# Performance work log

Hardware: AMD Instinct MI355X
Metric: run time of the kernel (lower is better)

Reference implementation:

```python
import jax, jax.numpy as jnp
import numpy as np

VOCAB, EMBED, HIDDEN, LAYERS = 256, 256, 1024, 2
B, T = 128, 256


def gru_layer(x_seq, h0, W_ih, W_hh, b_ih, b_hh):
    """PyTorch-semantics GRU layer. x_seq:[B,T,in], h0:[B,H] -> ([B,T,H], [B,H]).
    n = tanh(W_in x + b_in + r * (W_hn h + b_hn)); h' = (1-z)*n + z*h.
    Input-gate GEMM is hoisted out of the scan (one big matmul over all T)."""
    H = h0.shape[-1]
    gi = jnp.einsum('bti,gi->btg', x_seq, W_ih) + b_ih  # [B,T,3H]
    gi = jnp.transpose(gi, (1, 0, 2))                   # [T,B,3H] scan over time

    def step(h, gi_t):
        gh = h @ W_hh.T + b_hh                          # [B,3H]
        i_r, i_z, i_n = jnp.split(gi_t, 3, axis=-1)
        h_r, h_z, h_n = jnp.split(gh, 3, axis=-1)
        r = jax.nn.sigmoid(i_r + h_r)
        z = jax.nn.sigmoid(i_z + h_z)
        n = jnp.tanh(i_n + r * h_n)
        h_new = (1.0 - z) * n + z * h
        return h_new, h_new

    h_last, ys = jax.lax.scan(step, h0, gi)
    return jnp.transpose(ys, (1, 0, 2)), h_last         # [B,T,H], [B,H]


def setup_inputs() -> dict:
    key = jax.random.key(0)
    ks = jax.random.split(key, 16)
    s = 1.0 / np.sqrt(HIDDEN)
    u = lambda k, shape: jax.random.uniform(k, shape, jnp.float32, -s, s)
    inp = {
        'x': jax.random.randint(ks[0], (B, T), 0, VOCAB),
        'h0': jax.random.normal(ks[1], (LAYERS, B, HIDDEN), jnp.float32),
        'emb': jax.random.normal(ks[2], (VOCAB, EMBED), jnp.float32),
        'W_ih0': u(ks[3], (3 * HIDDEN, EMBED)),
        'W_hh0': u(ks[4], (3 * HIDDEN, HIDDEN)),
        'b_ih0': u(ks[5], (3 * HIDDEN,)),
        'b_hh0': u(ks[6], (3 * HIDDEN,)),
        'W_ih1': u(ks[7], (3 * HIDDEN, HIDDEN)),
        'W_hh1': u(ks[8], (3 * HIDDEN, HIDDEN)),
        'b_ih1': u(ks[9], (3 * HIDDEN,)),
        'b_hh1': u(ks[10], (3 * HIDDEN,)),
        'fc_W': u(ks[11], (VOCAB, HIDDEN)),
        'fc_b': u(ks[12], (VOCAB,)),
    }
    return inp


def reference(x, h0, emb, W_ih0, W_hh0, b_ih0, b_hh0, W_ih1, W_hh1, b_ih1, b_hh1, fc_W, fc_b):
    xe = emb[x]                                          # [B,T,E]
    y0, h_last0 = gru_layer(xe, h0[0], W_ih0, W_hh0, b_ih0, b_hh0)
    y1, h_last1 = gru_layer(y0, h0[1], W_ih1, W_hh1, b_ih1, b_hh1)
    logits = y1[:, -1, :] @ fc_W.T + fc_b                # [B,VOCAB]
    h = jnp.stack([h_last0, h_last1], axis=0)            # [LAYERS,B,H]
    return logits, h
```

## Files before the change

### kernel.cpp

```cpp
#include <hip/hip_runtime.h>
#include <hip/hip_bf16.h>

using bf16x8 = __attribute__((ext_vector_type(8))) __bf16;
using short8 = __attribute__((ext_vector_type(8))) short;
using f32x4  = __attribute__((ext_vector_type(4))) float;
using f4     = __attribute__((ext_vector_type(4))) float;
using i32x4  = __attribute__((ext_vector_type(4))) int;

constexpr int NB = 128;
constexpr int NT = 256;
constexpr int NH = 1024;
constexpr int NE = 256;
constexpr int NV = 256;

constexpr int WHH_BYTES = 48 * 2048;
constexpr int GH_FLOATS = 24 * 256;
constexpr int NBLK = 256;

__device__ __forceinline__ void ldg_sc(i32x4& d, const void* p) {
  asm volatile("global_load_dwordx4 %0, %1, off sc0 sc1" : "=v"(d) : "v"(p));
}
__device__ __forceinline__ void stg_sc(void* p, i32x4 v) {
  asm volatile("global_store_dwordx4 %0, %1, off sc0 sc1" :: "v"(p), "v"(v) : "memory");
}
__device__ __forceinline__ void vm0_fence() {
  asm volatile("s_waitcnt vmcnt(0)" ::: "memory");
}
__device__ __forceinline__ void use_dep(i32x4& d) {
  asm volatile("" : "+v"(d));
}

__device__ __forceinline__ bf16x8 cvt8(const float* p) {
  short8 r;
  #pragma unroll
  for (int j = 0; j < 8; ++j)
    r[j] = (short)__bfloat16_as_ushort(__float2bfloat16(p[j]));
  return __builtin_bit_cast(bf16x8, r);
}

__global__ __launch_bounds__(256) void embcvt_kernel(const float* __restrict__ e,
                                                     __hip_bfloat16* __restrict__ o) {
  int i = blockIdx.x * 256 + threadIdx.x;
  o[i] = __float2bfloat16(e[i]);
}

template<int LAYER>
__global__ __launch_bounds__(384) void gru_kernel(
    const int* __restrict__ x,
    const __hip_bfloat16* __restrict__ embb,
    const float* __restrict__ Wih,
    const float* __restrict__ Whh,
    const float* __restrict__ bih,
    const float* __restrict__ bhh,
    const float* __restrict__ h0,
    const __hip_bfloat16* __restrict__ yin,
    __hip_bfloat16* __restrict__ yout,
    __hip_bfloat16* __restrict__ hbuf,
    float* __restrict__ hout,
    unsigned int* __restrict__ flags)
{
  extern __shared__ char smem[];
  char*  sWhh  = smem;
  float* sGh   = (float*)(smem + WHH_BYTES);
  float* sBias = sGh + GH_FLOATS;
  char*  sH    = (char*)(sBias + 64);

  const int tid  = threadIdx.x;
  const int lane = tid & 63;
  const int wv   = tid >> 6;
  const int mt   = wv & 1;
  const int ks   = wv >> 1;
  const int b    = blockIdx.x;
  const int rb   = (b >> 1) & 3;
  const int cidx = (b & 1) * 32 + (b >> 3);
  const int r0   = rb * 32;
  const int c0   = cidx * 16;
  unsigned int* pf = flags + rb * 64 * 16;
  const int slot = cidx;
  const int l16  = lane & 15;
  const int lk8  = (lane >> 4) * 8;

  for (int it = 0; it < 16; ++it) {
    int idx = it * 384 + tid;
    int gr = idx >> 7, kc = idx & 127;
    int grow = (gr >> 4) * NH + c0 + (gr & 15);
    short8 v = __builtin_bit_cast(short8, cvt8(Whh + grow * NH + kc * 8));
    *(short8*)(sWhh + ((gr * 2048 + kc * 16) ^ ((gr & 7) << 4))) = v;
  }
  if (tid < 16)       sBias[tid] = bih[c0 + tid] + bhh[c0 + tid];
  else if (tid < 32)  { int c = NH + c0 + tid - 16;   sBias[tid] = bih[c] + bhh[c]; }
  else if (tid < 48)  { int c = 2*NH + c0 + tid - 32; sBias[tid] = bih[c]; }
  else if (tid < 64)  { int c = 2*NH + c0 + tid - 48; sBias[tid] = bhh[c]; }

  constexpr int NFRAG = (LAYER == 0) ? 8 : 32;
  constexpr int KIN   = (LAYER == 0) ? NE : NH;
  bf16x8 wreg[NFRAG];
  #pragma unroll
  for (int kf = 0; kf < NFRAG; ++kf) {
    int grow = ks * NH + c0 + l16;
    wreg[kf] = cvt8(Wih + grow * KIN + kf * 32 + lk8);
  }

  float hown[2] = {0.f, 0.f};
  #pragma unroll
  for (int ei = 0; ei < 2; ++ei) {
    int e = tid + ei * 384;
    if (e < 512) {
      float hv = h0[(r0 + (e >> 4)) * NH + c0 + (e & 15)];
      hown[ei] = hv;
      ((unsigned short*)sH)[e] = __bfloat16_as_ushort(__float2bfloat16(hv));
    }
  }
  __syncthreads();
  if (tid < 64) {
    i32x4 hv = *(const i32x4*)(sH + (tid >> 1) * 32 + (tid & 1) * 16);
    stg_sc(hbuf + (r0 + (tid >> 1)) * NH + c0 + (tid & 1) * 8, hv);
    vm0_fence();
    if (tid == 0)
      __hip_atomic_store(pf + slot * 16, 1u, __ATOMIC_RELAXED,
                         __HIP_MEMORY_SCOPE_AGENT);
  }

  for (int t = 0; t < NT; ++t) {
    const __hip_bfloat16* rbuf = hbuf + (t & 1) * (NB * NH);
    __hip_bfloat16* wbuf = hbuf + ((t + 1) & 1) * (NB * NH);
    const int arow = r0 + mt * 16 + l16;
    const int bxor = (l16 & 7) << 4;
    float* abase = sGh + (lane >> 4) * 64 + l16;

    constexpr int P1 = (LAYER == 0) ? 4 : 24;
    f32x4 ai = {0.f, 0.f, 0.f, 0.f};
    const __hip_bfloat16* xptr;
    if constexpr (LAYER == 0) {
      int xid = x[arow * NT + t];
      xptr = embb + xid * NE + lk8;
    } else {
      xptr = yin + (arow * NT + t) * NH + lk8;
    }
    #pragma unroll
    for (int kk = 0; kk < P1; ++kk) {
      bf16x8 a = __builtin_bit_cast(bf16x8, *(const short8*)(xptr + kk * 32));
      ai = __builtin_amdgcn_mfma_f32_16x16x32_bf16(a, wreg[kk], ai, 0, 0, 0);
    }

    {
      unsigned int ep = (unsigned int)(t + 1);
      if (tid < 64) {
        const unsigned int* f = pf + tid * 16;
        while (__hip_atomic_load(f, __ATOMIC_RELAXED,
                                 __HIP_MEMORY_SCOPE_AGENT) < ep)
          __builtin_amdgcn_s_sleep(1);
      }
      __syncthreads();
    }

    const int nk = (ks < 2) ? 11 : 10;
    const __hip_bfloat16* aptr = rbuf + arow * NH + lk8;
    i32x4 fr[11];
    #pragma unroll
    for (int i = 0; i < 11; ++i)
      if (i < nk) ldg_sc(fr[i], aptr + (ks + 3 * i) * 32);

    #pragma unroll
    for (int kk = P1; kk < NFRAG; ++kk) {
      bf16x8 a = __builtin_bit_cast(bf16x8, *(const short8*)(xptr + kk * 32));
      ai = __builtin_amdgcn_mfma_f32_16x16x32_bf16(a, wreg[kk], ai, 0, 0, 0);
    }
    {
      float* p = abase + (18 + mt * 3 + ks) * 256;
      p[0] = ai[0]; p[16] = ai[1]; p[32] = ai[2]; p[48] = ai[3];
    }

    vm0_fence();
    #pragma unroll
    for (int i = 0; i < 11; ++i)
      if (i < nk) use_dep(fr[i]);
    {
      f32x4 ah0 = {0.f,0.f,0.f,0.f}, ah1 = {0.f,0.f,0.f,0.f}, ah2 = {0.f,0.f,0.f,0.f};
      const int bb0 = (l16)      * 2048 + lk8 * 2;
      const int bb1 = (16 + l16) * 2048 + lk8 * 2;
      const int bb2 = (32 + l16) * 2048 + lk8 * 2;
      #pragma unroll
      for (int i = 0; i < 11; ++i) {
        if (i < nk) {
          int kk = ks + 3 * i;
          bf16x8 a = __builtin_bit_cast(bf16x8, fr[i]);
          bf16x8 b0 = __builtin_bit_cast(bf16x8,
              *(const short8*)(sWhh + ((bb0 + kk * 64) ^ bxor)));
          ah0 = __builtin_amdgcn_mfma_f32_16x16x32_bf16(a, b0, ah0, 0, 0, 0);
          bf16x8 b1 = __builtin_bit_cast(bf16x8,
              *(const short8*)(sWhh + ((bb1 + kk * 64) ^ bxor)));
          ah1 = __builtin_amdgcn_mfma_f32_16x16x32_bf16(a, b1, ah1, 0, 0, 0);
          bf16x8 b2 = __builtin_bit_cast(bf16x8,
              *(const short8*)(sWhh + ((bb2 + kk * 64) ^ bxor)));
          ah2 = __builtin_amdgcn_mfma_f32_16x16x32_bf16(a, b2, ah2, 0, 0, 0);
        }
      }
      float* p0 = abase + (ks * 6 + mt * 3 + 0) * 256;
      float* p1 = abase + (ks * 6 + mt * 3 + 1) * 256;
      float* p2 = abase + (ks * 6 + mt * 3 + 2) * 256;
      p0[0] = ah0[0]; p0[16] = ah0[1]; p0[32] = ah0[2]; p0[48] = ah0[3];
      p1[0] = ah1[0]; p1[16] = ah1[1]; p1[32] = ah1[2]; p1[48] = ah1[3];
      p2[0] = ah2[0]; p2[16] = ah2[1]; p2[32] = ah2[2]; p2[48] = ah2[3];
    }
    __syncthreads();

    #pragma unroll
    for (int ei = 0; ei < 2; ++ei) {
      int e = tid + ei * 384;
      if (e < 512) {
        int lrow = e >> 4, lcol = e & 15;
        int m2 = lrow >> 4, off = (lrow & 15) * 16 + lcol;
        float ghr = sGh[(0*6 + m2*3 + 0) * 256 + off]
                  + sGh[(1*6 + m2*3 + 0) * 256 + off]
                  + sGh[(2*6 + m2*3 + 0) * 256 + off];
        float ghz = sGh[(0*6 + m2*3 + 1) * 256 + off]
                  + sGh[(1*6 + m2*3 + 1) * 256 + off]
                  + sGh[(2*6 + m2*3 + 1) * 256 + off];
        float ghn = sGh[(0*6 + m2*3 + 2) * 256 + off]
                  + sGh[(1*6 + m2*3 + 2) * 256 + off]
                  + sGh[(2*6 + m2*3 + 2) * 256 + off];
        float gir = sGh[(18 + m2*3 + 0) * 256 + off];
        float giz = sGh[(18 + m2*3 + 1) * 256 + off];
        float gin = sGh[(18 + m2*3 + 2) * 256 + off];
        float r = 1.f / (1.f + __expf(-(gir + ghr + sBias[lcol])));
        float z = 1.f / (1.f + __expf(-(giz + ghz + sBias[16 + lcol])));
        float npre = (gin + sBias[32 + lcol]) + r * (ghn + sBias[48 + lcol]);
        float n = 2.f / (1.f + __expf(-2.f * npre)) - 1.f;
        float hn = (1.f - z) * n + z * hown[ei];
        hown[ei] = hn;
        __hip_bfloat16 hb = __float2bfloat16(hn);
        ((unsigned short*)sH)[e] = __bfloat16_as_ushort(hb);
        if constexpr (LAYER == 0)
          yout[((r0 + lrow) * NT + t) * NH + c0 + lcol] = hb;
      }
    }

    __syncthreads();
    if (tid < 64) {
      i32x4 hv = *(const i32x4*)(sH + (tid >> 1) * 32 + (tid & 1) * 16);
      stg_sc(wbuf + (r0 + (tid >> 1)) * NH + c0 + (tid & 1) * 8, hv);
      vm0_fence();
      if (tid == 0)
        __hip_atomic_store(pf + slot * 16, (unsigned int)(t + 2),
                           __ATOMIC_RELAXED, __HIP_MEMORY_SCOPE_AGENT);
    }
  }

  #pragma unroll
  for (int ei = 0; ei < 2; ++ei) {
    int e = tid + ei * 384;
    if (e < 512) {
      int lrow = e >> 4, lcol = e & 15;
      hout[(r0 + lrow) * NH + c0 + lcol] = hown[ei];
    }
  }
}

__global__ __launch_bounds__(256) void logits_kernel(
    const __hip_bfloat16* __restrict__ h1,
    const float* __restrict__ fcW,
    const float* __restrict__ fcb,
    float* __restrict__ out)
{
  __shared__ float hrow[NH];
  int b = blockIdx.x, v = threadIdx.x;
  if (v < 128) {
    i32x4 hv;
    ldg_sc(hv, h1 + b * NH + v * 8);
    vm0_fence();
    use_dep(hv);
    short8 s = __builtin_bit_cast(short8, hv);
    #pragma unroll
    for (int j = 0; j < 8; ++j) {
      union { unsigned int i; float f; } c;
      c.i = ((unsigned int)(unsigned short)s[j]) << 16;
      hrow[v * 8 + j] = c.f;
    }
  }
  __syncthreads();
  float acc = fcb[v];
  for (int k = 0; k < NH; k += 4) {
    f4 wv = *(const f4*)(fcW + v * NH + k);
    #pragma unroll
    for (int j = 0; j < 4; ++j) acc += wv[j] * hrow[k + j];
  }
  out[b * NV + v] = acc;
}

extern "C" void kernel_launch(void* const* d_in, const int* in_sizes, int n_in,
                              void* d_out, int out_size, void* d_ws, size_t ws_size,
                              hipStream_t stream) {
  const int*   x    = (const int*)d_in[0];
  const float* h0   = (const float*)d_in[1];
  const float* emb  = (const float*)d_in[2];
  const float* Wih0 = (const float*)d_in[3];
  const float* Whh0 = (const float*)d_in[4];
  const float* bih0 = (const float*)d_in[5];
  const float* bhh0 = (const float*)d_in[6];
  const float* Wih1 = (const float*)d_in[7];
  const float* Whh1 = (const float*)d_in[8];
  const float* bih1 = (const float*)d_in[9];
  const float* bhh1 = (const float*)d_in[10];
  const float* fcW  = (const float*)d_in[11];
  const float* fcb  = (const float*)d_in[12];
  float* out = (float*)d_out;

  char* ws = (char*)d_ws;
  size_t off = 0;
  __hip_bfloat16* y0   = (__hip_bfloat16*)ws;            off += (size_t)NB * NT * NH * 2;
  __hip_bfloat16* hbuf = (__hip_bfloat16*)(ws + off);    off += (size_t)2 * NB * NH * 2;
  __hip_bfloat16* embb = (__hip_bfloat16*)(ws + off);    off += (size_t)NV * NE * 2;
  unsigned int*  flags0 = (unsigned int*)(ws + off);     off += 4 * 64 * 16 * 4;
  unsigned int*  flags1 = (unsigned int*)(ws + off);     off += 4 * 64 * 16 * 4;

  (void)hipMemsetAsync(flags0, 0, 2 * 4 * 64 * 16 * 4, stream);
  embcvt_kernel<<<dim3(NV * NE / 256), dim3(256), 0, stream>>>(emb, embb);

  constexpr int lds = WHH_BYTES + GH_FLOATS * 4 + 64 * 4 + 1024;
  (void)hipFuncSetAttribute(reinterpret_cast<const void*>(gru_kernel<0>),
                            hipFuncAttributeMaxDynamicSharedMemorySize, lds);
  (void)hipFuncSetAttribute(reinterpret_cast<const void*>(gru_kernel<1>),
                            hipFuncAttributeMaxDynamicSharedMemorySize, lds);

  gru_kernel<0><<<dim3(NBLK), dim3(384), lds, stream>>>(
      x, embb, Wih0, Whh0, bih0, bhh0, h0, y0, y0, hbuf, out + 32768, flags0);
  gru_kernel<1><<<dim3(NBLK), dim3(384), lds, stream>>>(
      x, embb, Wih1, Whh1, bih1, bhh1, h0 + NB * NH, y0, y0, hbuf,
      out + 32768 + NB * NH, flags1);
  logits_kernel<<<dim3(NB), dim3(256), 0, stream>>>(hbuf, fcW, fcb, out);
}
```

Measured before the change: 4.082 ms.

## Restructure GRU cross-block sync with ballot polling, packed flags and direct h stores

Replaces the single-wave flag spin plus block barrier with per-wave ballot polling over packed (non-padded) flags. The wait is split so each wave first waits on the 32 blocks covering the first half of K and issues those loads early, then waits on the rest. Each thread now stores its bf16 hidden value straight to global memory, which removes the LDS staging step and its extra barrier. The input-gate r/z partials are folded into the hidden-gate accumulators, which shrinks the gate scratch area, and the layer-1 input prefetch split point moves. The aim is to cut the latency of the per-timestep grid synchronization, at the cost of many more small scattered global stores and more flag polling traffic from every wave.

Result: slower. 4.533 ms (+11.0%).

```diff
diff --git a/kernel.cpp b/kernel.cpp
--- a/kernel.cpp
+++ b/kernel.cpp
@@ -14,14 +14,14 @@
 constexpr int NV = 256;
 
 constexpr int WHH_BYTES = 48 * 2048;
-constexpr int GH_FLOATS = 24 * 256;
+constexpr int GH_FLOATS = 20 * 256;
 constexpr int NBLK = 256;
 
 __device__ __forceinline__ void ldg_sc(i32x4& d, const void* p) {
   asm volatile("global_load_dwordx4 %0, %1, off sc0 sc1" : "=v"(d) : "v"(p));
 }
-__device__ __forceinline__ void stg_sc(void* p, i32x4 v) {
-  asm volatile("global_store_dwordx4 %0, %1, off sc0 sc1" :: "v"(p), "v"(v) : "memory");
+__device__ __forceinline__ void stg_sc_u16(void* p, unsigned int v) {
+  asm volatile("global_store_short %0, %1, off sc0 sc1" :: "v"(p), "v"(v) : "memory");
 }
 __device__ __forceinline__ void vm0_fence() {
   asm volatile("s_waitcnt vmcnt(0)" ::: "memory");
@@ -45,7 +45,7 @@
 }
 
 template<int LAYER>
-__global__ __launch_bounds__(384) void gru_kernel(
+__global__ __launch_bounds__(384, 2) void gru_kernel(
     const int* __restrict__ x,
     const __hip_bfloat16* __restrict__ embb,
     const float* __restrict__ Wih,
@@ -63,7 +63,6 @@
   char*  sWhh  = smem;
   float* sGh   = (float*)(smem + WHH_BYTES);
   float* sBias = sGh + GH_FLOATS;
-  char*  sH    = (char*)(sBias + 64);
 
   const int tid  = threadIdx.x;
   const int lane = tid & 63;
@@ -75,7 +74,7 @@
   const int cidx = (b & 1) * 32 + (b >> 3);
   const int r0   = rb * 32;
   const int c0   = cidx * 16;
-  unsigned int* pf = flags + rb * 64 * 16;
+  unsigned int* pf = flags + rb * 64;
   const int slot = cidx;
   const int l16  = lane & 15;
   const int lk8  = (lane >> 4) * 8;
@@ -108,18 +107,15 @@
     if (e < 512) {
       float hv = h0[(r0 + (e >> 4)) * NH + c0 + (e & 15)];
       hown[ei] = hv;
-      ((unsigned short*)sH)[e] = __bfloat16_as_ushort(__float2bfloat16(hv));
-    }
-  }
+      unsigned int bits = (unsigned int)__bfloat16_as_ushort(__float2bfloat16(hv));
+      stg_sc_u16(hbuf + (r0 + (e >> 4)) * NH + c0 + (e & 15), bits);
+    }
+  }
+  vm0_fence();
   __syncthreads();
-  if (tid < 64) {
-    i32x4 hv = *(const i32x4*)(sH + (tid >> 1) * 32 + (tid & 1) * 16);
-    stg_sc(hbuf + (r0 + (tid >> 1)) * NH + c0 + (tid & 1) * 8, hv);
-    vm0_fence();
-    if (tid == 0)
-      __hip_atomic_store(pf + slot * 16, 1u, __ATOMIC_RELAXED,
-                         __HIP_MEMORY_SCOPE_AGENT);
-  }
+  if (tid == 0)
+    __hip_atomic_store(pf + slot, 1u, __ATOMIC_RELAXED,
+                       __HIP_MEMORY_SCOPE_AGENT);
 
   for (int t = 0; t < NT; ++t) {
     const __hip_bfloat16* rbuf = hbuf + (t & 1) * (NB * NH);
@@ -127,8 +123,9 @@
     const int arow = r0 + mt * 16 + l16;
     const int bxor = (l16 & 7) << 4;
     float* abase = sGh + (lane >> 4) * 64 + l16;
-
-    constexpr int P1 = (LAYER == 0) ? 4 : 24;
+    const unsigned int ep = (unsigned int)(t + 1);
+
+    constexpr int P1 = (LAYER == 0) ? 4 : 20;
     f32x4 ai = {0.f, 0.f, 0.f, 0.f};
     const __hip_bfloat16* xptr;
     if constexpr (LAYER == 0) {
@@ -144,37 +141,48 @@
     }
 
     {
-      unsigned int ep = (unsigned int)(t + 1);
-      if (tid < 64) {
-        const unsigned int* f = pf + tid * 16;
-        while (__hip_atomic_load(f, __ATOMIC_RELAXED,
-                                 __HIP_MEMORY_SCOPE_AGENT) < ep)
-          __builtin_amdgcn_s_sleep(1);
-      }
-      __syncthreads();
+      unsigned int fv = __hip_atomic_load(pf + lane, __ATOMIC_RELAXED,
+                                          __HIP_MEMORY_SCOPE_AGENT);
+      while ((__ballot(fv >= ep) & 0xFFFFFFFFull) != 0xFFFFFFFFull) {
+        __builtin_amdgcn_s_sleep(1);
+        fv = __hip_atomic_load(pf + lane, __ATOMIC_RELAXED,
+                               __HIP_MEMORY_SCOPE_AGENT);
+      }
     }
 
     const int nk = (ks < 2) ? 11 : 10;
+    const int n1 = (15 - ks) / 3 + 1;
     const __hip_bfloat16* aptr = rbuf + arow * NH + lk8;
     i32x4 fr[11];
     #pragma unroll
     for (int i = 0; i < 11; ++i)
-      if (i < nk) ldg_sc(fr[i], aptr + (ks + 3 * i) * 32);
+      if (i < n1) ldg_sc(fr[i], aptr + (ks + 3 * i) * 32);
 
     #pragma unroll
     for (int kk = P1; kk < NFRAG; ++kk) {
       bf16x8 a = __builtin_bit_cast(bf16x8, *(const short8*)(xptr + kk * 32));
       ai = __builtin_amdgcn_mfma_f32_16x16x32_bf16(a, wreg[kk], ai, 0, 0, 0);
     }
+
     {
-      float* p = abase + (18 + mt * 3 + ks) * 256;
-      p[0] = ai[0]; p[16] = ai[1]; p[32] = ai[2]; p[48] = ai[3];
-    }
+      unsigned int fv = __hip_atomic_load(pf + lane, __ATOMIC_RELAXED,
+                                          __HIP_MEMORY_SCOPE_AGENT);
+      while (__ballot(fv >= ep) != 0xFFFFFFFFFFFFFFFFull) {
+        __builtin_amdgcn_s_sleep(1);
+        fv = __hip_atomic_load(pf + lane, __ATOMIC_RELAXED,
+                               __HIP_MEMORY_SCOPE_AGENT);
+      }
+    }
+
+    #pragma unroll
+    for (int i = 0; i < 11; ++i)
+      if (i >= n1 && i < nk) ldg_sc(fr[i], aptr + (ks + 3 * i) * 32);
 
     vm0_fence();
     #pragma unroll
     for (int i = 0; i < 11; ++i)
       if (i < nk) use_dep(fr[i]);
+
     {
       f32x4 ah0 = {0.f,0.f,0.f,0.f}, ah1 = {0.f,0.f,0.f,0.f}, ah2 = {0.f,0.f,0.f,0.f};
       const int bb0 = (l16)      * 2048 + lk8 * 2;
@@ -196,12 +204,18 @@
           ah2 = __builtin_amdgcn_mfma_f32_16x16x32_bf16(a, b2, ah2, 0, 0, 0);
         }
       }
+      if (ks == 0)      ah0 += ai;
+      else if (ks == 1) ah1 += ai;
       float* p0 = abase + (ks * 6 + mt * 3 + 0) * 256;
       float* p1 = abase + (ks * 6 + mt * 3 + 1) * 256;
       float* p2 = abase + (ks * 6 + mt * 3 + 2) * 256;
       p0[0] = ah0[0]; p0[16] = ah0[1]; p0[32] = ah0[2]; p0[48] = ah0[3];
       p1[0] = ah1[0]; p1[16] = ah1[1]; p1[32] = ah1[2]; p1[48] = ah1[3];
       p2[0] = ah2[0]; p2[16] = ah2[1]; p2[32] = ah2[2]; p2[48] = ah2[3];
+      if (ks == 2) {
+        float* pi = abase + (18 + mt) * 256;
+        pi[0] = ai[0]; pi[16] = ai[1]; pi[32] = ai[2]; pi[48] = ai[3];
+      }
     }
     __syncthreads();
 
@@ -211,40 +225,35 @@
       if (e < 512) {
         int lrow = e >> 4, lcol = e & 15;
         int m2 = lrow >> 4, off = (lrow & 15) * 16 + lcol;
-        float ghr = sGh[(0*6 + m2*3 + 0) * 256 + off]
-                  + sGh[(1*6 + m2*3 + 0) * 256 + off]
-                  + sGh[(2*6 + m2*3 + 0) * 256 + off];
-        float ghz = sGh[(0*6 + m2*3 + 1) * 256 + off]
-                  + sGh[(1*6 + m2*3 + 1) * 256 + off]
-                  + sGh[(2*6 + m2*3 + 1) * 256 + off];
-        float ghn = sGh[(0*6 + m2*3 + 2) * 256 + off]
-                  + sGh[(1*6 + m2*3 + 2) * 256 + off]
-                  + sGh[(2*6 + m2*3 + 2) * 256 + off];
-        float gir = sGh[(18 + m2*3 + 0) * 256 + off];
-        float giz = sGh[(18 + m2*3 + 1) * 256 + off];
-        float gin = sGh[(18 + m2*3 + 2) * 256 + off];
-        float r = 1.f / (1.f + __expf(-(gir + ghr + sBias[lcol])));
-        float z = 1.f / (1.f + __expf(-(giz + ghz + sBias[16 + lcol])));
+        float ghr = sGh[(0 + m2*3 + 0) * 256 + off]
+                  + sGh[(6 + m2*3 + 0) * 256 + off]
+                  + sGh[(12 + m2*3 + 0) * 256 + off];
+        float ghz = sGh[(0 + m2*3 + 1) * 256 + off]
+                  + sGh[(6 + m2*3 + 1) * 256 + off]
+                  + sGh[(12 + m2*3 + 1) * 256 + off];
+        float ghn = sGh[(0 + m2*3 + 2) * 256 + off]
+                  + sGh[(6 + m2*3 + 2) * 256 + off]
+                  + sGh[(12 + m2*3 + 2) * 256 + off];
+        float gin = sGh[(18 + m2) * 256 + off];
+        float r = 1.f / (1.f + __expf(-(ghr + sBias[lcol])));
+        float z = 1.f / (1.f + __expf(-(ghz + sBias[16 + lcol])));
         float npre = (gin + sBias[32 + lcol]) + r * (ghn + sBias[48 + lcol]);
         float n = 2.f / (1.f + __expf(-2.f * npre)) - 1.f;
         float hn = (1.f - z) * n + z * hown[ei];
         hown[ei] = hn;
         __hip_bfloat16 hb = __float2bfloat16(hn);
-        ((unsigned short*)sH)[e] = __bfloat16_as_ushort(hb);
+        unsigned int bits = (unsigned int)__bfloat16_as_ushort(hb);
+        stg_sc_u16(wbuf + (r0 + lrow) * NH + c0 + lcol, bits);
         if constexpr (LAYER == 0)
           yout[((r0 + lrow) * NT + t) * NH + c0 + lcol] = hb;
       }
     }
 
+    vm0_fence();
     __syncthreads();
-    if (tid < 64) {
-      i32x4 hv = *(const i32x4*)(sH + (tid >> 1) * 32 + (tid & 1) * 16);
-      stg_sc(wbuf + (r0 + (tid >> 1)) * NH + c0 + (tid & 1) * 8, hv);
-      vm0_fence();
-      if (tid == 0)
-        __hip_atomic_store(pf + slot * 16, (unsigned int)(t + 2),
-                           __ATOMIC_RELAXED, __HIP_MEMORY_SCOPE_AGENT);
-    }
+    if (tid == 0)
+      __hip_atomic_store(pf + slot, (unsigned int)(t + 2),
+                         __ATOMIC_RELAXED, __HIP_MEMORY_SCOPE_AGENT);
   }
 
   #pragma unroll
@@ -311,13 +320,13 @@
   __hip_bfloat16* y0   = (__hip_bfloat16*)ws;            off += (size_t)NB * NT * NH * 2;
   __hip_bfloat16* hbuf = (__hip_bfloat16*)(ws + off);    off += (size_t)2 * NB * NH * 2;
   __hip_bfloat16* embb = (__hip_bfloat16*)(ws + off);    off += (size_t)NV * NE * 2;
-  unsigned int*  flags0 = (unsigned int*)(ws + off);     off += 4 * 64 * 16 * 4;
-  unsigned int*  flags1 = (unsigned int*)(ws + off);     off += 4 * 64 * 16 * 4;
-
-  (void)hipMemsetAsync(flags0, 0, 2 * 4 * 64 * 16 * 4, stream);
+  unsigned int*  flags0 = (unsigned int*)(ws + off);     off += 4 * 64 * 4;
+  unsigned int*  flags1 = (unsigned int*)(ws + off);     off += 4 * 64 * 4;
+
+  (void)hipMemsetAsync(flags0, 0, 2 * 4 * 64 * 4, stream);
   embcvt_kernel<<<dim3(NV * NE / 256), dim3(256), 0, stream>>>(emb, embb);
 
-  constexpr int lds = WHH_BYTES + GH_FLOATS * 4 + 64 * 4 + 1024;
+  constexpr int lds = WHH_BYTES + GH_FLOATS * 4 + 64 * 4;
   (void)hipFuncSetAttribute(reinterpret_cast<const void*>(gru_kernel<0>),
                             hipFuncAttributeMaxDynamicSharedMemorySize, lds);
   (void)hipFuncSetAttribute(reinterpret_cast<const void*>(gru_kernel<1>),
```

## Add dedicated flag-polling wave and split input GEMM by K halves

Applied to the files above, without the earlier changes.

Adds a seventh wave per block that only polls the peer-ready flags and publishes the new hidden state, so the six compute waves finish the full input-projection GEMM before the barrier instead of splitting it around the spin loop. The input GEMM is re-partitioned so each wave covers both 16-row tiles over half of K, with the two partial sums reduced in LDS during the gate phase. The hidden-state fragment loads are also rotated per block to spread global reads across addresses. This costs extra LDS for the partial sums and one more wave per block, and may add register pressure from the halved-K weight fragments and the duplicated accumulators.

New measurement: 4.752 ms. +16.4%, slower.

```diff
diff --git a/kernel.cpp b/kernel.cpp
--- a/kernel.cpp
+++ b/kernel.cpp
@@ -14,7 +14,7 @@
 constexpr int NV = 256;
 
 constexpr int WHH_BYTES = 48 * 2048;
-constexpr int GH_FLOATS = 24 * 256;
+constexpr int GH_FLOATS = 30 * 256;
 constexpr int NBLK = 256;
 
 __device__ __forceinline__ void ldg_sc(i32x4& d, const void* p) {
@@ -45,7 +45,7 @@
 }
 
 template<int LAYER>
-__global__ __launch_bounds__(384) void gru_kernel(
+__global__ __launch_bounds__(448, 2) void gru_kernel(
     const int* __restrict__ x,
     const __hip_bfloat16* __restrict__ embb,
     const float* __restrict__ Wih,
@@ -80,31 +80,35 @@
   const int l16  = lane & 15;
   const int lk8  = (lane >> 4) * 8;
 
-  for (int it = 0; it < 16; ++it) {
-    int idx = it * 384 + tid;
-    int gr = idx >> 7, kc = idx & 127;
-    int grow = (gr >> 4) * NH + c0 + (gr & 15);
-    short8 v = __builtin_bit_cast(short8, cvt8(Whh + grow * NH + kc * 8));
-    *(short8*)(sWhh + ((gr * 2048 + kc * 16) ^ ((gr & 7) << 4))) = v;
+  for (int it = 0; it < 14; ++it) {
+    int idx = it * 448 + tid;
+    if (idx < 6144) {
+      int gr = idx >> 7, kc = idx & 127;
+      int grow = (gr >> 4) * NH + c0 + (gr & 15);
+      short8 v = __builtin_bit_cast(short8, cvt8(Whh + grow * NH + kc * 8));
+      *(short8*)(sWhh + ((gr * 2048 + kc * 16) ^ ((gr & 7) << 4))) = v;
+    }
   }
   if (tid < 16)       sBias[tid] = bih[c0 + tid] + bhh[c0 + tid];
   else if (tid < 32)  { int c = NH + c0 + tid - 16;   sBias[tid] = bih[c] + bhh[c]; }
   else if (tid < 48)  { int c = 2*NH + c0 + tid - 32; sBias[tid] = bih[c]; }
   else if (tid < 64)  { int c = 2*NH + c0 + tid - 48; sBias[tid] = bhh[c]; }
 
-  constexpr int NFRAG = (LAYER == 0) ? 8 : 32;
   constexpr int KIN   = (LAYER == 0) ? NE : NH;
+  constexpr int NFRAG = KIN / 64;
   bf16x8 wreg[NFRAG];
-  #pragma unroll
-  for (int kf = 0; kf < NFRAG; ++kf) {
-    int grow = ks * NH + c0 + l16;
-    wreg[kf] = cvt8(Wih + grow * KIN + kf * 32 + lk8);
+  if (wv < 6) {
+    #pragma unroll
+    for (int kf = 0; kf < NFRAG; ++kf) {
+      int grow = ks * NH + c0 + l16;
+      wreg[kf] = cvt8(Wih + grow * KIN + mt * (KIN / 2) + kf * 32 + lk8);
+    }
   }
 
   float hown[2] = {0.f, 0.f};
   #pragma unroll
   for (int ei = 0; ei < 2; ++ei) {
-    int e = tid + ei * 384;
+    int e = tid + ei * 448;
     if (e < 512) {
       float hv = h0[(r0 + (e >> 4)) * NH + c0 + (e & 15)];
       hown[ei] = hv;
@@ -112,11 +116,11 @@
     }
   }
   __syncthreads();
-  if (tid < 64) {
-    i32x4 hv = *(const i32x4*)(sH + (tid >> 1) * 32 + (tid & 1) * 16);
-    stg_sc(hbuf + (r0 + (tid >> 1)) * NH + c0 + (tid & 1) * 8, hv);
+  if (wv == 6) {
+    i32x4 hv = *(const i32x4*)(sH + (lane >> 1) * 32 + (lane & 1) * 16);
+    stg_sc(hbuf + (r0 + (lane >> 1)) * NH + c0 + (lane & 1) * 8, hv);
     vm0_fence();
-    if (tid == 0)
+    if (lane == 0)
       __hip_atomic_store(pf + slot * 16, 1u, __ATOMIC_RELAXED,
                          __HIP_MEMORY_SCOPE_AGENT);
   }
@@ -124,58 +128,61 @@
   for (int t = 0; t < NT; ++t) {
     const __hip_bfloat16* rbuf = hbuf + (t & 1) * (NB * NH);
     __hip_bfloat16* wbuf = hbuf + ((t + 1) & 1) * (NB * NH);
-    const int arow = r0 + mt * 16 + l16;
     const int bxor = (l16 & 7) << 4;
     float* abase = sGh + (lane >> 4) * 64 + l16;
 
-    constexpr int P1 = (LAYER == 0) ? 4 : 24;
-    f32x4 ai = {0.f, 0.f, 0.f, 0.f};
-    const __hip_bfloat16* xptr;
-    if constexpr (LAYER == 0) {
-      int xid = x[arow * NT + t];
-      xptr = embb + xid * NE + lk8;
+    f32x4 ai0 = {0.f,0.f,0.f,0.f}, ai1 = {0.f,0.f,0.f,0.f};
+    if (wv < 6) {
+      #pragma unroll
+      for (int m = 0; m < 2; ++m) {
+        const __hip_bfloat16* xp;
+        if constexpr (LAYER == 0) {
+          int xid = x[(r0 + m * 16 + l16) * NT + t];
+          xp = embb + xid * NE + mt * (KIN / 2) + lk8;
+        } else {
+          xp = yin + ((r0 + m * 16 + l16) * NT + t) * NH + mt * (KIN / 2) + lk8;
+        }
+        f32x4 acc = {0.f,0.f,0.f,0.f};
+        #pragma unroll
+        for (int kf = 0; kf < NFRAG; ++kf) {
+          bf16x8 a = __builtin_bit_cast(bf16x8, *(const short8*)(xp + kf * 32));
+          acc = __builtin_amdgcn_mfma_f32_16x16x32_bf16(a, wreg[kf], acc, 0, 0, 0);
+        }
+        if (m == 0) ai0 = acc; else ai1 = acc;
+      }
     } else {
-      xptr = yin + (arow * NT + t) * NH + lk8;
-    }
-    #pragma unroll
-    for (int kk = 0; kk < P1; ++kk) {
-      bf16x8 a = __builtin_bit_cast(bf16x8, *(const short8*)(xptr + kk * 32));
-      ai = __builtin_amdgcn_mfma_f32_16x16x32_bf16(a, wreg[kk], ai, 0, 0, 0);
-    }
-
-    {
       unsigned int ep = (unsigned int)(t + 1);
-      if (tid < 64) {
-        const unsigned int* f = pf + tid * 16;
-        while (__hip_atomic_load(f, __ATOMIC_RELAXED,
-                                 __HIP_MEMORY_SCOPE_AGENT) < ep)
-          __builtin_amdgcn_s_sleep(1);
+      const unsigned int* f = pf + lane * 16;
+      while (__hip_atomic_load(f, __ATOMIC_RELAXED,
+                               __HIP_MEMORY_SCOPE_AGENT) < ep)
+        __builtin_amdgcn_s_sleep(1);
+    }
+    __syncthreads();
+
+    if (wv < 6) {
+      float* pi0 = abase + (18 + (ks * 2 + mt) * 2 + 0) * 256;
+      float* pi1 = abase + (18 + (ks * 2 + mt) * 2 + 1) * 256;
+      pi0[0]=ai0[0]; pi0[16]=ai0[1]; pi0[32]=ai0[2]; pi0[48]=ai0[3];
+      pi1[0]=ai1[0]; pi1[16]=ai1[1]; pi1[32]=ai1[2]; pi1[48]=ai1[3];
+
+      const int nk = (ks < 2) ? 11 : 10;
+      const int rot = cidx % nk;
+      const __hip_bfloat16* aptr = rbuf + (r0 + mt * 16 + l16) * NH + lk8;
+      i32x4 fr[11];
+      int kks[11];
+      #pragma unroll
+      for (int i = 0; i < 11; ++i) {
+        if (i < nk) {
+          int j = i + rot; if (j >= nk) j -= nk;
+          kks[i] = ks + 3 * j;
+          ldg_sc(fr[i], aptr + kks[i] * 32);
+        }
       }
-      __syncthreads();
-    }
-
-    const int nk = (ks < 2) ? 11 : 10;
-    const __hip_bfloat16* aptr = rbuf + arow * NH + lk8;
-    i32x4 fr[11];
-    #pragma unroll
-    for (int i = 0; i < 11; ++i)
-      if (i < nk) ldg_sc(fr[i], aptr + (ks + 3 * i) * 32);
-
-    #pragma unroll
-    for (int kk = P1; kk < NFRAG; ++kk) {
-      bf16x8 a = __builtin_bit_cast(bf16x8, *(const short8*)(xptr + kk * 32));
-      ai = __builtin_amdgcn_mfma_f32_16x16x32_bf16(a, wreg[kk], ai, 0, 0, 0);
-    }
-    {
-      float* p = abase + (18 + mt * 3 + ks) * 256;
-      p[0] = ai[0]; p[16] = ai[1]; p[32] = ai[2]; p[48] = ai[3];
-    }
-
-    vm0_fence();
-    #pragma unroll
-    for (int i = 0; i < 11; ++i)
-      if (i < nk) use_dep(fr[i]);
-    {
+      vm0_fence();
+      #pragma unroll
+      for (int i = 0; i < 11; ++i)
+        if (i < nk) use_dep(fr[i]);
+
       f32x4 ah0 = {0.f,0.f,0.f,0.f}, ah1 = {0.f,0.f,0.f,0.f}, ah2 = {0.f,0.f,0.f,0.f};
       const int bb0 = (l16)      * 2048 + lk8 * 2;
       const int bb1 = (16 + l16) * 2048 + lk8 * 2;
@@ -183,7 +190,7 @@
       #pragma unroll
       for (int i = 0; i < 11; ++i) {
         if (i < nk) {
-          int kk = ks + 3 * i;
+          int kk = kks[i];
           bf16x8 a = __builtin_bit_cast(bf16x8, fr[i]);
           bf16x8 b0 = __builtin_bit_cast(bf16x8,
               *(const short8*)(sWhh + ((bb0 + kk * 64) ^ bxor)));
@@ -199,15 +206,15 @@
       float* p0 = abase + (ks * 6 + mt * 3 + 0) * 256;
       float* p1 = abase + (ks * 6 + mt * 3 + 1) * 256;
       float* p2 = abase + (ks * 6 + mt * 3 + 2) * 256;
-      p0[0] = ah0[0]; p0[16] = ah0[1]; p0[32] = ah0[2]; p0[48] = ah0[3];
-      p1[0] = ah1[0]; p1[16] = ah1[1]; p1[32] = ah1[2]; p1[48] = ah1[3];
-      p2[0] = ah2[0]; p2[16] = ah2[1]; p2[32] = ah2[2]; p2[48] = ah2[3];
+      p0[0]=ah0[0]; p0[16]=ah0[1]; p0[32]=ah0[2]; p0[48]=ah0[3];
+      p1[0]=ah1[0]; p1[16]=ah1[1]; p1[32]=ah1[2]; p1[48]=ah1[3];
+      p2[0]=ah2[0]; p2[16]=ah2[1]; p2[32]=ah2[2]; p2[48]=ah2[3];
     }
     __syncthreads();
 
     #pragma unroll
     for (int ei = 0; ei < 2; ++ei) {
-      int e = tid + ei * 384;
+      int e = tid + ei * 448;
       if (e < 512) {
         int lrow = e >> 4, lcol = e & 15;
         int m2 = lrow >> 4, off = (lrow & 15) * 16 + lcol;
@@ -220,9 +227,12 @@
         float ghn = sGh[(0*6 + m2*3 + 2) * 256 + off]
                   + sGh[(1*6 + m2*3 + 2) * 256 + off]
                   + sGh[(2*6 + m2*3 + 2) * 256 + off];
-        float gir = sGh[(18 + m2*3 + 0) * 256 + off];
-        float giz = sGh[(18 + m2*3 + 1) * 256 + off];
-        float gin = sGh[(18 + m2*3 + 2) * 256 + off];
+        float gir = sGh[(18 + 0*2 + 0) * 256 + off] + sGh[(18 + 1*2 + 0) * 256 + off];
+        float giz = sGh[(18 + 2*2 + 0) * 256 + off] + sGh[(18 + 3*2 + 0) * 256 + off];
+        float gin = sGh[(18 + 4*2 + 0) * 256 + off] + sGh[(18 + 5*2 + 0) * 256 + off];
+        gir = sGh[(18 + (0*2+0)*2 + m2) * 256 + off] + sGh[(18 + (0*2+1)*2 + m2) * 256 + off];
+        giz = sGh[(18 + (1*2+0)*2 + m2) * 256 + off] + sGh[(18 + (1*2+1)*2 + m2) * 256 + off];
+        gin = sGh[(18 + (2*2+0)*2 + m2) * 256 + off] + sGh[(18 + (2*2+1)*2 + m2) * 256 + off];
         float r = 1.f / (1.f + __expf(-(gir + ghr + sBias[lcol])));
         float z = 1.f / (1.f + __expf(-(giz + ghz + sBias[16 + lcol])));
         float npre = (gin + sBias[32 + lcol]) + r * (ghn + sBias[48 + lcol]);
@@ -235,13 +245,13 @@
           yout[((r0 + lrow) * NT + t) * NH + c0 + lcol] = hb;
       }
     }
-
     __syncthreads();
-    if (tid < 64) {
-      i32x4 hv = *(const i32x4*)(sH + (tid >> 1) * 32 + (tid & 1) * 16);
-      stg_sc(wbuf + (r0 + (tid >> 1)) * NH + c0 + (tid & 1) * 8, hv);
+
+    if (wv == 6) {
+      i32x4 hv = *(const i32x4*)(sH + (lane >> 1) * 32 + (lane & 1) * 16);
+      stg_sc(wbuf + (r0 + (lane >> 1)) * NH + c0 + (lane & 1) * 8, hv);
       vm0_fence();
-      if (tid == 0)
+      if (lane == 0)
         __hip_atomic_store(pf + slot * 16, (unsigned int)(t + 2),
                            __ATOMIC_RELAXED, __HIP_MEMORY_SCOPE_AGENT);
     }
@@ -249,7 +259,7 @@
 
   #pragma unroll
   for (int ei = 0; ei < 2; ++ei) {
-    int e = tid + ei * 384;
+    int e = tid + ei * 448;
     if (e < 512) {
       int lrow = e >> 4, lcol = e & 15;
       hout[(r0 + lrow) * NH + c0 + lcol] = hown[ei];
@@ -323,9 +333,9 @@
   (void)hipFuncSetAttribute(reinterpret_cast<const void*>(gru_kernel<1>),
                             hipFuncAttributeMaxDynamicSharedMemorySize, lds);
 
-  gru_kernel<0><<<dim3(NBLK), dim3(384), lds, stream>>>(
+  gru_kernel<0><<<dim3(NBLK), dim3(448), lds, stream>>>(
       x, embb, Wih0, Whh0, bih0, bhh0, h0, y0, y0, hbuf, out + 32768, flags0);
-  gru_kernel<1><<<dim3(NBLK), dim3(384), lds, stream>>>(
+  gru_kernel<1><<<dim3(NBLK), dim3(448), lds, stream>>>(
       x, embb, Wih1, Whh1, bih1, bhh1, h0 + NB * NH, y0, y0, hbuf,
       out + 32768 + NB * NH, flags1);
   logits_kernel<<<dim3(NB), dim3(256), 0, stream>>>(hbuf, fcW, fcb, out);
```

## Split input-gate GEMM over K halves to halve weight registers per wave

Applied to the files above, without the earlier changes.

Each wave now holds only half of the K dimension of its W_ih slice in registers and computes the input-gate partial products for both 16-row M tiles, instead of the full K for one tile. The two K-half partials are written to extra shared-memory slots and summed in the gate update, which enlarges the shared buffer. Launch bounds now request two blocks per SM, aiming to cut register pressure and spilling in layer 1. The cost is extra shared-memory traffic and an additional reduction add per gate.

Result: faster. 3.933 ms (-3.6%).

```diff
diff --git a/kernel.cpp b/kernel.cpp
--- a/kernel.cpp
+++ b/kernel.cpp
@@ -14,7 +14,7 @@
 constexpr int NV = 256;
 
 constexpr int WHH_BYTES = 48 * 2048;
-constexpr int GH_FLOATS = 24 * 256;
+constexpr int GH_FLOATS = 30 * 256;
 constexpr int NBLK = 256;
 
 __device__ __forceinline__ void ldg_sc(i32x4& d, const void* p) {
@@ -45,7 +45,7 @@
 }
 
 template<int LAYER>
-__global__ __launch_bounds__(384) void gru_kernel(
+__global__ __launch_bounds__(384, 2) void gru_kernel(
     const int* __restrict__ x,
     const __hip_bfloat16* __restrict__ embb,
     const float* __restrict__ Wih,
@@ -92,13 +92,14 @@
   else if (tid < 48)  { int c = 2*NH + c0 + tid - 32; sBias[tid] = bih[c]; }
   else if (tid < 64)  { int c = 2*NH + c0 + tid - 48; sBias[tid] = bhh[c]; }
 
-  constexpr int NFRAG = (LAYER == 0) ? 8 : 32;
   constexpr int KIN   = (LAYER == 0) ? NE : NH;
+  constexpr int NFRAG = KIN / 64;
+  const int khalf = mt * (KIN / 2);
   bf16x8 wreg[NFRAG];
   #pragma unroll
   for (int kf = 0; kf < NFRAG; ++kf) {
     int grow = ks * NH + c0 + l16;
-    wreg[kf] = cvt8(Wih + grow * KIN + kf * 32 + lk8);
+    wreg[kf] = cvt8(Wih + grow * KIN + khalf + kf * 32 + lk8);
   }
 
   float hown[2] = {0.f, 0.f};
@@ -128,19 +129,19 @@
     const int bxor = (l16 & 7) << 4;
     float* abase = sGh + (lane >> 4) * 64 + l16;
 
-    constexpr int P1 = (LAYER == 0) ? 4 : 24;
-    f32x4 ai = {0.f, 0.f, 0.f, 0.f};
-    const __hip_bfloat16* xptr;
+    f32x4 ai0 = {0.f,0.f,0.f,0.f}, ai1 = {0.f,0.f,0.f,0.f};
+    const __hip_bfloat16 *xp0, *xp1;
     if constexpr (LAYER == 0) {
-      int xid = x[arow * NT + t];
-      xptr = embb + xid * NE + lk8;
+      xp0 = embb + x[(r0 + l16) * NT + t] * NE + khalf + lk8;
+      xp1 = embb + x[(r0 + 16 + l16) * NT + t] * NE + khalf + lk8;
     } else {
-      xptr = yin + (arow * NT + t) * NH + lk8;
-    }
-    #pragma unroll
-    for (int kk = 0; kk < P1; ++kk) {
-      bf16x8 a = __builtin_bit_cast(bf16x8, *(const short8*)(xptr + kk * 32));
-      ai = __builtin_amdgcn_mfma_f32_16x16x32_bf16(a, wreg[kk], ai, 0, 0, 0);
+      xp0 = yin + ((r0 + l16) * NT + t) * NH + khalf + lk8;
+      xp1 = yin + ((r0 + 16 + l16) * NT + t) * NH + khalf + lk8;
+    }
+    #pragma unroll
+    for (int kf = 0; kf < NFRAG; ++kf) {
+      bf16x8 a = __builtin_bit_cast(bf16x8, *(const short8*)(xp0 + kf * 32));
+      ai0 = __builtin_amdgcn_mfma_f32_16x16x32_bf16(a, wreg[kf], ai0, 0, 0, 0);
     }
 
     {
@@ -162,13 +163,15 @@
       if (i < nk) ldg_sc(fr[i], aptr + (ks + 3 * i) * 32);
 
     #pragma unroll
-    for (int kk = P1; kk < NFRAG; ++kk) {
-      bf16x8 a = __builtin_bit_cast(bf16x8, *(const short8*)(xptr + kk * 32));
-      ai = __builtin_amdgcn_mfma_f32_16x16x32_bf16(a, wreg[kk], ai, 0, 0, 0);
+    for (int kf = 0; kf < NFRAG; ++kf) {
+      bf16x8 a = __builtin_bit_cast(bf16x8, *(const short8*)(xp1 + kf * 32));
+      ai1 = __builtin_amdgcn_mfma_f32_16x16x32_bf16(a, wreg[kf], ai1, 0, 0, 0);
     }
     {
-      float* p = abase + (18 + mt * 3 + ks) * 256;
-      p[0] = ai[0]; p[16] = ai[1]; p[32] = ai[2]; p[48] = ai[3];
+      float* pi0 = abase + (18 + (ks * 2 + mt) * 2 + 0) * 256;
+      float* pi1 = abase + (18 + (ks * 2 + mt) * 2 + 1) * 256;
+      pi0[0]=ai0[0]; pi0[16]=ai0[1]; pi0[32]=ai0[2]; pi0[48]=ai0[3];
+      pi1[0]=ai1[0]; pi1[16]=ai1[1]; pi1[32]=ai1[2]; pi1[48]=ai1[3];
     }
 
     vm0_fence();
@@ -199,9 +202,9 @@
       float* p0 = abase + (ks * 6 + mt * 3 + 0) * 256;
       float* p1 = abase + (ks * 6 + mt * 3 + 1) * 256;
       float* p2 = abase + (ks * 6 + mt * 3 + 2) * 256;
-      p0[0] = ah0[0]; p0[16] = ah0[1]; p0[32] = ah0[2]; p0[48] = ah0[3];
-      p1[0] = ah1[0]; p1[16] = ah1[1]; p1[32] = ah1[2]; p1[48] = ah1[3];
-      p2[0] = ah2[0]; p2[16] = ah2[1]; p2[32] = ah2[2]; p2[48] = ah2[3];
+      p0[0]=ah0[0]; p0[16]=ah0[1]; p0[32]=ah0[2]; p0[48]=ah0[3];
+      p1[0]=ah1[0]; p1[16]=ah1[1]; p1[32]=ah1[2]; p1[48]=ah1[3];
+      p2[0]=ah2[0]; p2[16]=ah2[1]; p2[32]=ah2[2]; p2[48]=ah2[3];
     }
     __syncthreads();
 
@@ -220,9 +223,12 @@
         float ghn = sGh[(0*6 + m2*3 + 2) * 256 + off]
                   + sGh[(1*6 + m2*3 + 2) * 256 + off]
                   + sGh[(2*6 + m2*3 + 2) * 256 + off];
-        float gir = sGh[(18 + m2*3 + 0) * 256 + off];
-        float giz = sGh[(18 + m2*3 + 1) * 256 + off];
-        float gin = sGh[(18 + m2*3 + 2) * 256 + off];
+        float gir = sGh[(18 + (0*2+0)*2 + m2) * 256 + off]
+                  + sGh[(18 + (0*2+1)*2 + m2) * 256 + off];
+        float giz = sGh[(18 + (1*2+0)*2 + m2) * 256 + off]
+                  + sGh[(18 + (1*2+1)*2 + m2) * 256 + off];
+        float gin = sGh[(18 + (2*2+0)*2 + m2) * 256 + off]
+                  + sGh[(18 + (2*2+1)*2 + m2) * 256 + off];
         float r = 1.f / (1.f + __expf(-(gir + ghr + sBias[lcol])));
         float z = 1.f / (1.f + __expf(-(giz + ghz + sBias[16 + lcol])));
         float npre = (gin + sBias[32 + lcol]) + r * (ghn + sBias[48 + lcol]);
```
